# Optimization experiments

Hardware: AMD Instinct MI355X
Metric: run time of the kernel (lower is better)

Reference implementation:

```python
import jax, jax.numpy as jnp
import numpy as np

DIM = 2048
N_HEADS = 16
N_KV_HEADS = 8
HEAD_DIM = DIM // N_HEADS  # 128
N_REP = N_HEADS // N_KV_HEADS
BATCH = 2
SEQ = 2048
CHUNK = 128  # chunked-parallel causal linear attention; SEQ % CHUNK == 0


def _make_freqs_cis(seq_len, head_dim, theta=10000.0):
    freqs = 1.0 / (theta ** (np.arange(0, head_dim, 2, dtype=np.float32) / head_dim))
    t = np.arange(seq_len, dtype=np.float32)
    ang = np.outer(t, freqs)  # [S, D/2]
    return jnp.asarray(np.stack([np.cos(ang), np.sin(ang)], axis=-1))  # [S, D/2, 2]


def setup_inputs() -> dict:
    key = jax.random.key(0)
    ks = jax.random.split(key, 5)
    x = jax.random.normal(ks[0], (BATCH, SEQ, DIM), dtype=jnp.float32)
    freqs_cis = _make_freqs_cis(SEQ, HEAD_DIM)
    s = 0.02
    wq = s * jax.random.normal(ks[1], (N_HEADS * HEAD_DIM, DIM), dtype=jnp.float32)
    wk = s * jax.random.normal(ks[2], (N_KV_HEADS * HEAD_DIM, DIM), dtype=jnp.float32)
    wv = s * jax.random.normal(ks[3], (N_KV_HEADS * HEAD_DIM, DIM), dtype=jnp.float32)
    wo = s * jax.random.normal(ks[4], (DIM, N_HEADS * HEAD_DIM), dtype=jnp.float32)
    return {"x": x, "freqs_cis": freqs_cis, "wq": wq, "wk": wk, "wv": wv, "wo": wo}


def _apply_rotary(x, freqs_cis):
    # x: [B, S, H, D]; freqs_cis: [S, D/2, 2] (cos, sin). Llama pairing: (x0,x1),(x2,x3),...
    B, S, H, D = x.shape
    xr = x.reshape(B, S, H, D // 2, 2)
    x0, x1 = xr[..., 0], xr[..., 1]
    c = freqs_cis[None, :, None, :, 0]
    s = freqs_cis[None, :, None, :, 1]
    o0 = x0 * c - x1 * s
    o1 = x0 * s + x1 * c
    return jnp.stack([o0, o1], axis=-1).reshape(B, S, H, D)


def _causal_linear_attention(q, k, v):
    # q, k, v: [B, H, S, D]; output_i = q_i @ sum_{j<=i} k_j^T v_j
    B, H, S, D = q.shape
    q = jax.nn.softmax(q * (D ** -0.5), axis=-1)  # softmax over feature dim
    k = jax.nn.softmax(k, axis=2)                 # softmax over sequence dim (as in source)
    Nc = S // CHUNK
    qc = q.reshape(B, H, Nc, CHUNK, D)
    kc = k.reshape(B, H, Nc, CHUNK, D)
    vc = v.reshape(B, H, Nc, CHUNK, D)
    # per-chunk KV outer-product sums: [B, H, Nc, D, D]
    kv = jnp.einsum('bhncd,bhnce->bhnde', kc, vc)
    cum = jnp.cumsum(kv, axis=2)
    cum_excl = jnp.concatenate([jnp.zeros_like(cum[:, :, :1]), cum[:, :, :-1]], axis=2)
    inter = jnp.einsum('bhncd,bhnde->bhnce', qc, cum_excl)
    scores = jnp.einsum('bhncd,bhnmd->bhncm', qc, kc)  # [B,H,Nc,C,C]
    mask = jnp.tril(jnp.ones((CHUNK, CHUNK), dtype=bool))
    scores = jnp.where(mask, scores, jnp.zeros((), dtype=scores.dtype))
    intra = jnp.einsum('bhncm,bhnme->bhnce', scores, vc)
    return (inter + intra).reshape(B, H, S, D)


def reference(x, freqs_cis, wq, wk, wv, wo):
    B, S, _ = x.shape
    xq = (x @ wq.T).reshape(B, S, N_HEADS, HEAD_DIM)
    xk = (x @ wk.T).reshape(B, S, N_KV_HEADS, HEAD_DIM)
    xv = (x @ wv.T).reshape(B, S, N_KV_HEADS, HEAD_DIM)
    xq = _apply_rotary(xq, freqs_cis)
    xk = _apply_rotary(xk, freqs_cis)
    # repeat_kv: each kv head repeated N_REP consecutive times
    keys = jnp.repeat(xk, N_REP, axis=2)
    values = jnp.repeat(xv, N_REP, axis=2)
    q = jnp.transpose(xq, (0, 2, 1, 3))
    k = jnp.transpose(keys, (0, 2, 1, 3))
    v = jnp.transpose(values, (0, 2, 1, 3))
    out = _causal_linear_attention(q, k, v)  # [B, H, S, D]
    out = jnp.transpose(out, (0, 2, 1, 3)).reshape(B, S, N_HEADS * HEAD_DIM)
    return out @ wo.T
```

## Files before the change

kernel.cpp:

```cpp
#include <hip/hip_runtime.h>
#include <math.h>

#define DIMV 2048
#define NHEAD 16
#define NKV 8
#define HD 128
#define BATCH 2
#define SEQ 2048
#define CHUNK 128
#define NCHUNK 16
#define MTOK 4096
#define KVD (NKV * HD)

typedef _Float16 half8_t __attribute__((ext_vector_type(8)));
typedef _Float16 half4_t __attribute__((ext_vector_type(4)));
typedef _Float16 half2_t __attribute__((ext_vector_type(2)));
typedef float f32x4 __attribute__((ext_vector_type(4)));

#define GLOBAL_AS __attribute__((address_space(1)))
#define LDS_AS __attribute__((address_space(3)))

__global__ __launch_bounds__(256) void cast_all(const float* __restrict__ x,
                                                const float* __restrict__ wq,
                                                const float* __restrict__ wk,
                                                const float* __restrict__ wv,
                                                const float* __restrict__ wo,
                                                _Float16* __restrict__ xh,
                                                _Float16* __restrict__ wqkvh,
                                                _Float16* __restrict__ woh) {
  long i = (long)(blockIdx.x * 256 + threadIdx.x) * 8;
  const float* src;
  _Float16* dst;
  long off;
  if (i < 8388608)        { src = x;  dst = xh;              off = 0; }
  else if (i < 12582912)  { src = wq; dst = wqkvh;           off = 8388608; }
  else if (i < 14680064)  { src = wk; dst = wqkvh + 4194304; off = 12582912; }
  else if (i < 16777216)  { src = wv; dst = wqkvh + 6291456; off = 14680064; }
  else                    { src = wo; dst = woh;             off = 16777216; }
  long e = i - off;
  float4 a = *(const float4*)&src[e];
  float4 b = *(const float4*)&src[e + 4];
  half8_t h = {(_Float16)a.x, (_Float16)a.y, (_Float16)a.z, (_Float16)a.w,
               (_Float16)b.x, (_Float16)b.y, (_Float16)b.z, (_Float16)b.w};
  *(half8_t*)&dst[e] = h;
}

__global__ __launch_bounds__(256) void transpose_fc(const float* __restrict__ fc,
                                                    float* __restrict__ fcT) {
  __shared__ float T[64][65];
  int s0 = blockIdx.x * 64, d0 = blockIdx.y * 64;
  int t = threadIdx.x;
  int r = t >> 4, c4 = (t & 15) * 4;
#pragma unroll
  for (int p = 0; p < 4; ++p) {
    int sr = p * 16 + r;
    float4 v = *(const float4*)&fc[(size_t)(s0 + sr) * 128 + d0 + c4];
    T[sr][c4] = v.x; T[sr][c4 + 1] = v.y; T[sr][c4 + 2] = v.z; T[sr][c4 + 3] = v.w;
  }
  __syncthreads();
#pragma unroll
  for (int p = 0; p < 4; ++p) {
    int dr = p * 16 + r;
    float4 v = make_float4(T[c4][dr], T[c4 + 1][dr], T[c4 + 2][dr], T[c4 + 3][dr]);
    *(float4*)&fcT[(size_t)(d0 + dr) * SEQ + s0 + c4] = v;
  }
}

__global__ __launch_bounds__(256) void hgemm_qkv(const _Float16* __restrict__ A,
                                                 const _Float16* __restrict__ B,
                                                 const float* __restrict__ fc,
                                                 _Float16* __restrict__ qh,
                                                 _Float16* __restrict__ kT,
                                                 _Float16* __restrict__ vT) {
  const int K = 2048;
  __shared__ _Float16 As[128 * 64];
  __shared__ _Float16 Bs[128 * 64];
  __shared__ float qsum[2][128];
  const int tid = threadIdx.x;
  const int lane = tid & 63;
  const int wave = tid >> 6;
  const int row0 = blockIdx.y * 128, col0 = blockIdx.x * 128;
  const int wr = wave & 1, wc = wave >> 1;
  const int m16 = lane & 15, quad = lane >> 4;

  f32x4 acc[4][4];
#pragma unroll
  for (int i = 0; i < 4; ++i)
#pragma unroll
    for (int j = 0; j < 4; ++j) acc[i][j] = (f32x4){0.f, 0.f, 0.f, 0.f};

  const int r_ld = tid >> 3;
  const int sseg = (tid & 7) ^ (r_ld & 7);
  const size_t a_base = (size_t)(row0 + r_ld) * K + sseg * 8;
  const size_t b_base = (size_t)(col0 + r_ld) * K + sseg * 8;
  _Float16* ldsA = As + wave * 512;
  _Float16* ldsB = Bs + wave * 512;
  const int swzA = quad ^ (m16 & 7);

  for (int k0 = 0; k0 < K; k0 += 64) {
#pragma unroll
    for (int i = 0; i < 4; ++i) {
      __builtin_amdgcn_global_load_lds(
          (const GLOBAL_AS void*)(A + a_base + (size_t)i * 32 * K + k0),
          (LDS_AS void*)(ldsA + i * 2048), 16, 0, 0);
      __builtin_amdgcn_global_load_lds(
          (const GLOBAL_AS void*)(B + b_base + (size_t)i * 32 * K + k0),
          (LDS_AS void*)(ldsB + i * 2048), 16, 0, 0);
    }
    __syncthreads();
#pragma unroll
    for (int kk = 0; kk < 2; ++kk) {
      const int swz = swzA ^ (kk * 4);
      half8_t af[4], bf[4];
#pragma unroll
      for (int i = 0; i < 4; ++i) {
        af[i] = *(half8_t*)&As[(wr * 64 + i * 16 + m16) * 64 + swz * 8];
        bf[i] = *(half8_t*)&Bs[(wc * 64 + i * 16 + m16) * 64 + swz * 8];
      }
#pragma unroll
      for (int i = 0; i < 4; ++i)
#pragma unroll
        for (int j = 0; j < 4; ++j)
          acc[i][j] = __builtin_amdgcn_mfma_f32_16x16x32_f16(af[i], bf[j], acc[i][j], 0, 0, 0);
    }
    __syncthreads();
  }

  if (col0 < 2048) {
    const float sc = 0.08838834764831845f;
    float psum[4][4];
#pragma unroll
    for (int i = 0; i < 4; ++i)
#pragma unroll
      for (int r = 0; r < 4; ++r) psum[i][r] = 0.f;
#pragma unroll
    for (int i = 0; i < 4; ++i)
#pragma unroll
      for (int j = 0; j < 4; ++j) {
        int dl2 = (wc * 64 + j * 16 + m16) & ~1;
#pragma unroll
        for (int r = 0; r < 4; ++r) {
          float val = acc[i][j][r];
          float par = __shfl_xor(val, 1);
          int s_tok = (row0 + wr * 64 + i * 16 + quad * 4 + r) & (SEQ - 1);
          float2 cs = *(const float2*)&fc[(size_t)s_tok * 128 + dl2];
          float o = val * cs.x + par * ((m16 & 1) ? cs.y : -cs.y);
          float e = __expf(o * sc);
          acc[i][j][r] = e;
          psum[i][r] += e;
        }
      }
#pragma unroll
    for (int m = 1; m < 16; m <<= 1)
#pragma unroll
      for (int i = 0; i < 4; ++i)
#pragma unroll
        for (int r = 0; r < 4; ++r) psum[i][r] += __shfl_xor(psum[i][r], m);
    if (m16 == 0) {
#pragma unroll
      for (int i = 0; i < 4; ++i)
#pragma unroll
        for (int r = 0; r < 4; ++r)
          qsum[wc][wr * 64 + i * 16 + quad * 4 + r] = psum[i][r];
    }
    __syncthreads();
#pragma unroll
    for (int i = 0; i < 4; ++i)
#pragma unroll
      for (int r = 0; r < 4; ++r) {
        int rowl = wr * 64 + i * 16 + quad * 4 + r;
        psum[i][r] = 1.f / (qsum[0][rowl] + qsum[1][rowl]);
      }
#pragma unroll
    for (int i = 0; i < 4; ++i)
#pragma unroll
      for (int j = 0; j < 4; ++j) {
        int col = col0 + wc * 64 + j * 16 + m16;
#pragma unroll
        for (int r = 0; r < 4; ++r) {
          int row = row0 + wr * 64 + i * 16 + quad * 4 + r;
          qh[(size_t)row * DIMV + col] = (_Float16)(acc[i][j][r] * psum[i][r]);
        }
      }
  } else {
#pragma unroll
    for (int i = 0; i < 4; ++i)
#pragma unroll
      for (int j = 0; j < 4; ++j) {
        int col = col0 + wc * 64 + j * 16 + m16;
        int rowb = row0 + wr * 64 + i * 16 + quad * 4;
        half4_t hv = {(_Float16)acc[i][j][0], (_Float16)acc[i][j][1],
                      (_Float16)acc[i][j][2], (_Float16)acc[i][j][3]};
        if (col0 < 3072) {
          *(half4_t*)&kT[(size_t)(col - 2048) * MTOK + rowb] = hv;
        } else {
          *(half4_t*)&vT[(size_t)(col - 3072) * MTOK + rowb] = hv;
        }
      }
  }
}

__global__ __launch_bounds__(256) void hgemm_bt64_f32(const _Float16* __restrict__ A,
                                                      const _Float16* __restrict__ B,
                                                      float* __restrict__ C,
                                                      int M, int N, int K) {
  __shared__ _Float16 As[128 * 64];
  __shared__ _Float16 Bs[128 * 64];
  const int tid = threadIdx.x;
  const int lane = tid & 63;
  const int wave = tid >> 6;
  const int row0 = blockIdx.y * 128, col0 = blockIdx.x * 128;
  const int wr = wave & 1, wc = wave >> 1;
  const int m16 = lane & 15, quad = lane >> 4;

  f32x4 acc[4][4];
#pragma unroll
  for (int i = 0; i < 4; ++i)
#pragma unroll
    for (int j = 0; j < 4; ++j) acc[i][j] = (f32x4){0.f, 0.f, 0.f, 0.f};

  const int r_ld = tid >> 3;
  const int sseg = (tid & 7) ^ (r_ld & 7);
  const size_t a_base = (size_t)(row0 + r_ld) * K + sseg * 8;
  const size_t b_base = (size_t)(col0 + r_ld) * K + sseg * 8;
  _Float16* ldsA = As + wave * 512;
  _Float16* ldsB = Bs + wave * 512;
  const int swzA = quad ^ (m16 & 7);

  for (int k0 = 0; k0 < K; k0 += 64) {
#pragma unroll
    for (int i = 0; i < 4; ++i) {
      __builtin_amdgcn_global_load_lds(
          (const GLOBAL_AS void*)(A + a_base + (size_t)i * 32 * K + k0),
          (LDS_AS void*)(ldsA + i * 2048), 16, 0, 0);
      __builtin_amdgcn_global_load_lds(
          (const GLOBAL_AS void*)(B + b_base + (size_t)i * 32 * K + k0),
          (LDS_AS void*)(ldsB + i * 2048), 16, 0, 0);
    }
    __syncthreads();
#pragma unroll
    for (int kk = 0; kk < 2; ++kk) {
      const int swz = swzA ^ (kk * 4);
      half8_t af[4], bf[4];
#pragma unroll
      for (int i = 0; i < 4; ++i) {
        af[i] = *(half8_t*)&As[(wr * 64 + i * 16 + m16) * 64 + swz * 8];
        bf[i] = *(half8_t*)&Bs[(wc * 64 + i * 16 + m16) * 64 + swz * 8];
      }
#pragma unroll
      for (int i = 0; i < 4; ++i)
#pragma unroll
        for (int j = 0; j < 4; ++j)
          acc[i][j] = __builtin_amdgcn_mfma_f32_16x16x32_f16(af[i], bf[j], acc[i][j], 0, 0, 0);
    }
    __syncthreads();
  }

#pragma unroll
  for (int i = 0; i < 4; ++i)
#pragma unroll
    for (int j = 0; j < 4; ++j) {
      int col = col0 + wc * 64 + j * 16 + m16;
      int rowb = row0 + wr * 64 + i * 16 + quad * 4;
#pragma unroll
      for (int r = 0; r < 4; ++r) C[(size_t)(rowb + r) * N + col] = acc[i][j][r];
    }
}

__global__ __launch_bounds__(256) void k_rope_softmax_T(_Float16* __restrict__ kT,
                                                        const float* __restrict__ fcT) {
  int bi = blockIdx.x;
  int b = bi & 1, pr = bi >> 1;
  int d0 = pr * 2, dl = d0 & 127;
  int t = threadIdx.x;
  size_t r0 = (size_t)d0 * MTOK + b * SEQ + t * 8;
  size_t r1 = r0 + MTOK;
  half8_t x0v = *(half8_t*)&kT[r0];
  half8_t x1v = *(half8_t*)&kT[r1];
  int s8 = t * 8;
  float4 ca = *(const float4*)&fcT[(size_t)dl * SEQ + s8];
  float4 cb = *(const float4*)&fcT[(size_t)dl * SEQ + s8 + 4];
  float4 sa = *(const float4*)&fcT[(size_t)(dl + 1) * SEQ + s8];
  float4 sb = *(const float4*)&fcT[(size_t)(dl + 1) * SEQ + s8 + 4];
  float cc[8] = {ca.x, ca.y, ca.z, ca.w, cb.x, cb.y, cb.z, cb.w};
  float ss[8] = {sa.x, sa.y, sa.z, sa.w, sb.x, sb.y, sb.z, sb.w};
  float e0[8], e1[8];
  float sum0 = 0.f, sum1 = 0.f;
#pragma unroll
  for (int j = 0; j < 8; ++j) {
    float x0 = (float)x0v[j], x1 = (float)x1v[j];
    float o0 = x0 * cc[j] - x1 * ss[j];
    float o1 = x0 * ss[j] + x1 * cc[j];
    e0[j] = expf(o0); e1[j] = expf(o1);
    sum0 += e0[j]; sum1 += e1[j];
  }
#pragma unroll
  for (int off = 1; off < 64; off <<= 1) {
    sum0 += __shfl_xor(sum0, off);
    sum1 += __shfl_xor(sum1, off);
  }
  __shared__ float red[8];
  if ((t & 63) == 0) { red[(t >> 6) * 2] = sum0; red[(t >> 6) * 2 + 1] = sum1; }
  __syncthreads();
  float S0 = red[0] + red[2] + red[4] + red[6];
  float S1 = red[1] + red[3] + red[5] + red[7];
  float i0 = 1.f / S0, i1 = 1.f / S1;
  half8_t w0, w1;
#pragma unroll
  for (int j = 0; j < 8; ++j) {
    w0[j] = (_Float16)(e0[j] * i0);
    w1[j] = (_Float16)(e1[j] * i1);
  }
  *(half8_t*)&kT[r0] = w0;
  *(half8_t*)&kT[r1] = w1;
}

__global__ __launch_bounds__(256) void transpose_k(const _Float16* __restrict__ kT,
                                                   _Float16* __restrict__ kh) {
  __shared__ _Float16 T[64][65];
  int t0 = blockIdx.x * 64, d0 = blockIdx.y * 64;
  int t = threadIdx.x;
  int r = t >> 3, c8 = (t & 7) * 8;
#pragma unroll
  for (int p = 0; p < 2; ++p) {
    int dr = p * 32 + r;
    half8_t v = *(const half8_t*)&kT[(size_t)(d0 + dr) * MTOK + t0 + c8];
#pragma unroll
    for (int j = 0; j < 8; ++j) T[c8 + j][dr] = v[j];
  }
  __syncthreads();
#pragma unroll
  for (int p = 0; p < 2; ++p) {
    int tr = p * 32 + r;
    half8_t v;
#pragma unroll
    for (int j = 0; j < 8; ++j) v[j] = T[tr][c8 + j];
    *(half8_t*)&kh[(size_t)(t0 + tr) * KVD + d0 + c8] = v;
  }
}

__global__ __launch_bounds__(256) void kv_chunk_mfma(const _Float16* __restrict__ vT,
                                                     const _Float16* __restrict__ kT,
                                                     float* __restrict__ kvT) {
  __shared__ _Float16 As[128 * 32];
  __shared__ _Float16 Bs[128 * 32];
  int bi = blockIdx.x;
  int n = bi & 15, kvh = (bi >> 4) & 7, b = bi >> 7;
  int tok0 = b * SEQ + n * CHUNK;
  const int tid = threadIdx.x;
  const int lane = tid & 63;
  const int wave = tid >> 6;
  const int wr = wave & 1, wc = wave >> 1;
  const int m16 = lane & 15, quad = lane >> 4;

  f32x4 acc[4][4];
#pragma unroll
  for (int i = 0; i < 4; ++i)
#pragma unroll
    for (int j = 0; j < 4; ++j) acc[i][j] = (f32x4){0.f, 0.f, 0.f, 0.f};

  const int r_ld = tid >> 2;
  const int seg = tid & 3;
  const size_t a_base = (size_t)(kvh * HD + r_ld) * MTOK + tok0 + seg * 8;
  const size_t b_base = a_base;
  _Float16* ldsA = As + wave * 512;
  _Float16* ldsB = Bs + wave * 512;

  for (int k0 = 0; k0 < 128; k0 += 32) {
#pragma unroll
    for (int i = 0; i < 2; ++i) {
      __builtin_amdgcn_global_load_lds(
          (const GLOBAL_AS void*)(vT + a_base + (size_t)i * 64 * MTOK + k0),
          (LDS_AS void*)(ldsA + i * 2048), 16, 0, 0);
      __builtin_amdgcn_global_load_lds(
          (const GLOBAL_AS void*)(kT + b_base + (size_t)i * 64 * MTOK + k0),
          (LDS_AS void*)(ldsB + i * 2048), 16, 0, 0);
    }
    __syncthreads();
    half8_t af[4], bf[4];
#pragma unroll
    for (int i = 0; i < 4; ++i) {
      af[i] = *(half8_t*)&As[(wr * 64 + i * 16 + m16) * 32 + quad * 8];
      bf[i] = *(half8_t*)&Bs[(wc * 64 + i * 16 + m16) * 32 + quad * 8];
    }
#pragma unroll
    for (int i = 0; i < 4; ++i)
#pragma unroll
      for (int j = 0; j < 4; ++j)
        acc[i][j] = __builtin_amdgcn_mfma_f32_16x16x32_f16(af[i], bf[j], acc[i][j], 0, 0, 0);
    __syncthreads();
  }
#pragma unroll
  for (int i = 0; i < 4; ++i)
#pragma unroll
    for (int j = 0; j < 4; ++j) {
      int col = wc * 64 + j * 16 + m16;
      int rowb = wr * 64 + i * 16 + quad * 4;
#pragma unroll
      for (int r = 0; r < 4; ++r)
        kvT[(size_t)bi * 16384 + (size_t)(rowb + r) * 128 + col] = acc[i][j][r];
    }
}

__global__ __launch_bounds__(256) void cumsum_h(const float* __restrict__ kvT,
                                                _Float16* __restrict__ cumh) {
  int gid = blockIdx.x * 256 + threadIdx.x;
  int bk = gid >> 14, idx = gid & 16383;
  size_t base = (size_t)bk * NCHUNK * 16384 + idx;
  float run = 0.f;
#pragma unroll
  for (int n = 0; n < NCHUNK; ++n) {
    cumh[base + (size_t)n * 16384] = (_Float16)run;
    run += kvT[base + (size_t)n * 16384];
  }
}

__global__ __launch_bounds__(256) void attn_fused(const _Float16* __restrict__ qh,
                                                  const _Float16* __restrict__ kh,
                                                  const _Float16* __restrict__ cumh,
                                                  const _Float16* __restrict__ vT,
                                                  _Float16* __restrict__ ath) {
  __shared__ _Float16 As[128 * 32];
  __shared__ _Float16 Bs[128 * 32];
  __shared__ _Float16 Ss[128][136];
  int bi = blockIdx.x;
  int n = bi & 15, h = (bi >> 4) & 15, b = bi >> 8;
  int kvh = h >> 1;
  int tok0 = b * SEQ + n * CHUNK;
  const int tid = threadIdx.x;
  const int lane = tid & 63;
  const int wave = tid >> 6;
  const int wr = wave & 1, wc = wave >> 1;
  const int m16 = lane & 15, quad = lane >> 4;
  const int r_ld = tid >> 2;
  const int seg = tid & 3;
  _Float16* ldsA = As + wave * 512;
  _Float16* ldsB = Bs + wave * 512;

  f32x4 acc[4][4];
#pragma unroll
  for (int i = 0; i < 4; ++i)
#pragma unroll
    for (int j = 0; j < 4; ++j) acc[i][j] = (f32x4){0.f, 0.f, 0.f, 0.f};

  const size_t qbase = (size_t)(tok0 + r_ld) * DIMV + h * HD + seg * 8;
  const size_t kbase = (size_t)(tok0 + r_ld) * KVD + kvh * HD + seg * 8;
  const size_t cbase = ((size_t)((b * 8 + kvh) * 16 + n)) * 16384 + (size_t)r_ld * 128 + seg * 8;
  const size_t vbase = (size_t)(kvh * HD + r_ld) * MTOK + tok0 + seg * 8;

  for (int k0 = 0; k0 < 128; k0 += 32) {
#pragma unroll
    for (int i = 0; i < 2; ++i) {
      __builtin_amdgcn_global_load_lds(
          (const GLOBAL_AS void*)(qh + qbase + (size_t)i * 64 * DIMV + k0),
          (LDS_AS void*)(ldsA + i * 2048), 16, 0, 0);
      __builtin_amdgcn_global_load_lds(
          (const GLOBAL_AS void*)(kh + kbase + (size_t)i * 64 * KVD + k0),
          (LDS_AS void*)(ldsB + i * 2048), 16, 0, 0);
    }
    __syncthreads();
    half8_t af[4], bf[4];
#pragma unroll
    for (int i = 0; i < 4; ++i) {
      af[i] = *(half8_t*)&As[(wr * 64 + i * 16 + m16) * 32 + quad * 8];
      bf[i] = *(half8_t*)&Bs[(wc * 64 + i * 16 + m16) * 32 + quad * 8];
    }
#pragma unroll
    for (int i = 0; i < 4; ++i)
#pragma unroll
      for (int j = 0; j < 4; ++j)
        acc[i][j] = __builtin_amdgcn_mfma_f32_16x16x32_f16(af[i], bf[j], acc[i][j], 0, 0, 0);
    __syncthreads();
  }

#pragma unroll
  for (int i = 0; i < 4; ++i)
#pragma unroll
    for (int j = 0; j < 4; ++j) {
      int col = wc * 64 + j * 16 + m16;
      int rowb = wr * 64 + i * 16 + quad * 4;
#pragma unroll
      for (int r = 0; r < 4; ++r) {
        float v = (col <= rowb + r) ? acc[i][j][r] : 0.f;
        Ss[rowb + r][col] = (_Float16)v;
      }
      acc[i][j] = (f32x4){0.f, 0.f, 0.f, 0.f};
    }

  for (int ks = 0; ks < 4; ++ks) {
    int k0 = ks * 32;
#pragma unroll
    for (int i = 0; i < 2; ++i) {
      __builtin_amdgcn_global_load_lds(
          (const GLOBAL_AS void*)(qh + qbase + (size_t)i * 64 * DIMV + k0),
          (LDS_AS void*)(ldsA + i * 2048), 16, 0, 0);
      __builtin_amdgcn_global_load_lds(
          (const GLOBAL_AS void*)(cumh + cbase + (size_t)i * 64 * 128 + k0),
          (LDS_AS void*)(ldsB + i * 2048), 16, 0, 0);
    }
    __syncthreads();
    half8_t af[4], bf[4];
#pragma unroll
    for (int i = 0; i < 4; ++i) {
      af[i] = *(half8_t*)&As[(wr * 64 + i * 16 + m16) * 32 + quad * 8];
      bf[i] = *(half8_t*)&Bs[(wc * 64 + i * 16 + m16) * 32 + quad * 8];
    }
#pragma unroll
    for (int i = 0; i < 4; ++i)
#pragma unroll
      for (int j = 0; j < 4; ++j)
        acc[i][j] = __builtin_amdgcn_mfma_f32_16x16x32_f16(af[i], bf[j], acc[i][j], 0, 0, 0);
    __syncthreads();
  }

  for (int ks = 0; ks < 4; ++ks) {
    int k0 = ks * 32;
#pragma unroll
    for (int i = 0; i < 2; ++i) {
      __builtin_amdgcn_global_load_lds(
          (const GLOBAL_AS void*)(vT + vbase + (size_t)i * 64 * MTOK + k0),
          (LDS_AS void*)(ldsB + i * 2048), 16, 0, 0);
    }
    __syncthreads();
    half8_t af[4], bf[4];
#pragma unroll
    for (int i = 0; i < 4; ++i) {
      af[i] = *(half8_t*)&Ss[wr * 64 + i * 16 + m16][k0 + quad * 8];
      bf[i] = *(half8_t*)&Bs[(wc * 64 + i * 16 + m16) * 32 + quad * 8];
    }
#pragma unroll
    for (int i = 0; i < 4; ++i)
#pragma unroll
      for (int j = 0; j < 4; ++j)
        acc[i][j] = __builtin_amdgcn_mfma_f32_16x16x32_f16(af[i], bf[j], acc[i][j], 0, 0, 0);
    __syncthreads();
  }

#pragma unroll
  for (int i = 0; i < 4; ++i)
#pragma unroll
    for (int j = 0; j < 4; ++j) {
      int col = wc * 64 + j * 16 + m16;
      int rowb = wr * 64 + i * 16 + quad * 4;
#pragma unroll
      for (int r = 0; r < 4; ++r)
        ath[(size_t)(tok0 + rowb + r) * DIMV + h * HD + col] = (_Float16)acc[i][j][r];
    }
}

extern "C" void kernel_launch(void* const* d_in, const int* in_sizes, int n_in,
                              void* d_out, int out_size, void* d_ws, size_t ws_size,
                              hipStream_t stream) {
  const float* x  = (const float*)d_in[0];
  const float* fc = (const float*)d_in[1];
  const float* wq = (const float*)d_in[2];
  const float* wk = (const float*)d_in[3];
  const float* wv = (const float*)d_in[4];
  const float* wo = (const float*)d_in[5];
  float* out = (float*)d_out;

  char* p = (char*)d_ws;
  _Float16* xh    = (_Float16*)p;  p += 16777216;
  _Float16* wqkvh = (_Float16*)p;  p += 16777216;
  _Float16* woh   = (_Float16*)p;  p += 8388608;
  _Float16* qh    = (_Float16*)p;  p += 16777216;
  _Float16* kT    = (_Float16*)p;  p += 8388608;
  _Float16* kh    = (_Float16*)p;  p += 8388608;
  _Float16* vT    = (_Float16*)p;  p += 8388608;
  float*    kvT   = (float*)p;     p += 16777216;
  _Float16* cumh  = (_Float16*)p;  p += 8388608;
  _Float16* ath   = (_Float16*)p;  p += 16777216;
  float*    fcT   = (float*)p;     p += 1048576;

  cast_all<<<10240, 256, 0, stream>>>(x, wq, wk, wv, wo, xh, wqkvh, woh);
  transpose_fc<<<dim3(32, 2), 256, 0, stream>>>(fc, fcT);

  hgemm_qkv<<<dim3(32, 32), 256, 0, stream>>>(xh, wqkvh, fc, qh, kT, vT);

  k_rope_softmax_T<<<1024, 256, 0, stream>>>(kT, fcT);
  transpose_k<<<dim3(64, 16), 256, 0, stream>>>(kT, kh);

  kv_chunk_mfma<<<256, 256, 0, stream>>>(vT, kT, kvT);
  cumsum_h<<<1024, 256, 0, stream>>>(kvT, cumh);
  attn_fused<<<512, 256, 0, stream>>>(qh, kh, cumh, vT, ath);

  hgemm_bt64_f32<<<dim3(16, 32), 256, 0, stream>>>(ath, woh, out, MTOK, 2048, 2048);
}
```

Measured before the change: 298.0 us.

## Rewrite QKV GEMM as 256x256 tile with 8-wave double-buffered ping-pong pipeline

```diff
diff --git a/kernel.cpp b/kernel.cpp
--- a/kernel.cpp
+++ b/kernel.cpp
@@ -66,131 +66,187 @@
   }
 }
 
-__global__ __launch_bounds__(256) void hgemm_qkv(const _Float16* __restrict__ A,
-                                                 const _Float16* __restrict__ B,
-                                                 const float* __restrict__ fc,
-                                                 _Float16* __restrict__ qh,
-                                                 _Float16* __restrict__ kT,
-                                                 _Float16* __restrict__ vT) {
+#define BARX() __builtin_amdgcn_s_barrier()
+#define WAITL0() asm volatile("s_waitcnt lgkmcnt(0)" ::: "memory")
+#define WAITVM(n) asm volatile("s_waitcnt vmcnt(" #n ")" ::: "memory")
+
+#define STG_A(bb, kk, i, k0)                                                      \
+  __builtin_amdgcn_global_load_lds(                                               \
+      (const GLOBAL_AS void*)(A + aoff + (size_t)(i) * 128 * 2048 + (k0) + (kk) * 32), \
+      (LDS_AS void*)(As + ((bb) * 2 + (kk)) * 8192 + (i) * 4096 + wave * 512), 16, 0, 0)
+#define STG_B(bb, kk, i, k0)                                                      \
+  __builtin_amdgcn_global_load_lds(                                               \
+      (const GLOBAL_AS void*)(B + boff + (size_t)(i) * 128 * 2048 + (k0) + (kk) * 32), \
+      (LDS_AS void*)(Bs + ((bb) * 2 + (kk)) * 8192 + (i) * 4096 + wave * 512), 16, 0, 0)
+
+#define LDA_F(bb, kk, ih) do {                                                    \
+    const _Float16* pA_ = As + ((bb) * 2 + (kk)) * 8192 +                         \
+                          (wr * 128 + (ih) * 64 + m16) * 32 + pseg8;              \
+    af[0] = *(const half8_t*)(pA_);                                               \
+    af[1] = *(const half8_t*)(pA_ + 512);                                         \
+    af[2] = *(const half8_t*)(pA_ + 1024);                                        \
+    af[3] = *(const half8_t*)(pA_ + 1536);                                        \
+  } while (0)
+#define LDB_F(bb, kk) do {                                                        \
+    const _Float16* pB_ = Bs + ((bb) * 2 + (kk)) * 8192 +                         \
+                          (wc * 64 + m16) * 32 + pseg8;                           \
+    bf[0] = *(const half8_t*)(pB_);                                               \
+    bf[1] = *(const half8_t*)(pB_ + 512);                                         \
+    bf[2] = *(const half8_t*)(pB_ + 1024);                                        \
+    bf[3] = *(const half8_t*)(pB_ + 1536);                                        \
+  } while (0)
+
+#define MMX(ih) do {                                                              \
+    _Pragma("unroll")                                                             \
+    for (int i_ = 0; i_ < 4; ++i_)                                                \
+      _Pragma("unroll")                                                           \
+      for (int j_ = 0; j_ < 4; ++j_)                                              \
+        acc[(ih) * 4 + i_][j_] = __builtin_amdgcn_mfma_f32_16x16x32_f16(          \
+            af[i_], bf[j_], acc[(ih) * 4 + i_][j_], 0, 0, 0);                     \
+  } while (0)
+
+#define KTILE(bb, k0, DS1, DS2, DS3, DS4, VA, VB) do {                            \
+  half8_t af[4], bf[4];                                                           \
+                                                           \
+  LDA_F(bb, 0, 0); LDB_F(bb, 0);                                                  \
+  if (DS1) { STG_A(1 - (bb), 1, 0, (k0) + 64); STG_A(1 - (bb), 1, 1, (k0) + 64); } \
+  BARX(); WAITL0();                                                               \
+  __builtin_amdgcn_s_setprio(1); MMX(0); __builtin_amdgcn_s_setprio(0);           \
+  BARX();                                                                         \
+                                                \
+  LDA_F(bb, 0, 1);                                                                \
+  if (DS2) { STG_B(1 - (bb), 1, 0, (k0) + 64); STG_B(1 - (bb), 1, 1, (k0) + 64); } \
+  WAITVM(VA);                                                                     \
+  BARX(); WAITL0();                                                               \
+  __builtin_amdgcn_s_setprio(1); MMX(1); __builtin_amdgcn_s_setprio(0);           \
+  BARX();                                                                         \
+                                                           \
+  LDA_F(bb, 1, 0); LDB_F(bb, 1);                                                  \
+  if (DS3) { STG_A(bb, 0, 0, (k0) + 128); STG_A(bb, 0, 1, (k0) + 128); }          \
+  BARX(); WAITL0();                                                               \
+  __builtin_amdgcn_s_setprio(1); MMX(0); __builtin_amdgcn_s_setprio(0);           \
+  BARX();                                                                         \
+                                                \
+  LDA_F(bb, 1, 1);                                                                \
+  if (DS4) { STG_B(bb, 0, 0, (k0) + 128); STG_B(bb, 0, 1, (k0) + 128); }          \
+  WAITVM(VB);                                                                     \
+  BARX(); WAITL0();                                                               \
+  __builtin_amdgcn_s_setprio(1); MMX(1); __builtin_amdgcn_s_setprio(0);           \
+  BARX();                                                                         \
+} while (0)
+
+__global__ __launch_bounds__(512, 2) void hgemm_qkv_8p(const _Float16* __restrict__ A,
+                                                       const _Float16* __restrict__ B,
+                                                       const float* __restrict__ fc,
+                                                       _Float16* __restrict__ qh,
+                                                       _Float16* __restrict__ kT,
+                                                       _Float16* __restrict__ vT) {
   const int K = 2048;
-  __shared__ _Float16 As[128 * 64];
-  __shared__ _Float16 Bs[128 * 64];
-  __shared__ float qsum[2][128];
+  __shared__ _Float16 As[32768];
+  __shared__ _Float16 Bs[32768];
+  __shared__ float qsum[4][256];
+
   const int tid = threadIdx.x;
   const int lane = tid & 63;
   const int wave = tid >> 6;
-  const int row0 = blockIdx.y * 128, col0 = blockIdx.x * 128;
-  const int wr = wave & 1, wc = wave >> 1;
+  const int wr = wave >> 2;
+  const int wc = wave & 3;
   const int m16 = lane & 15, quad = lane >> 4;
-
-  f32x4 acc[4][4];
-#pragma unroll
-  for (int i = 0; i < 4; ++i)
-#pragma unroll
-    for (int j = 0; j < 4; ++j) acc[i][j] = (f32x4){0.f, 0.f, 0.f, 0.f};
-
-  const int r_ld = tid >> 3;
-  const int sseg = (tid & 7) ^ (r_ld & 7);
-  const size_t a_base = (size_t)(row0 + r_ld) * K + sseg * 8;
-  const size_t b_base = (size_t)(col0 + r_ld) * K + sseg * 8;
-  _Float16* ldsA = As + wave * 512;
-  _Float16* ldsB = Bs + wave * 512;
-  const int swzA = quad ^ (m16 & 7);
-
-  for (int k0 = 0; k0 < K; k0 += 64) {
-#pragma unroll
-    for (int i = 0; i < 4; ++i) {
-      __builtin_amdgcn_global_load_lds(
-          (const GLOBAL_AS void*)(A + a_base + (size_t)i * 32 * K + k0),
-          (LDS_AS void*)(ldsA + i * 2048), 16, 0, 0);
-      __builtin_amdgcn_global_load_lds(
-          (const GLOBAL_AS void*)(B + b_base + (size_t)i * 32 * K + k0),
-          (LDS_AS void*)(ldsB + i * 2048), 16, 0, 0);
-    }
-    __syncthreads();
-#pragma unroll
-    for (int kk = 0; kk < 2; ++kk) {
-      const int swz = swzA ^ (kk * 4);
-      half8_t af[4], bf[4];
-#pragma unroll
-      for (int i = 0; i < 4; ++i) {
-        af[i] = *(half8_t*)&As[(wr * 64 + i * 16 + m16) * 64 + swz * 8];
-        bf[i] = *(half8_t*)&Bs[(wc * 64 + i * 16 + m16) * 64 + swz * 8];
-      }
-#pragma unroll
-      for (int i = 0; i < 4; ++i)
-#pragma unroll
-        for (int j = 0; j < 4; ++j)
-          acc[i][j] = __builtin_amdgcn_mfma_f32_16x16x32_f16(af[i], bf[j], acc[i][j], 0, 0, 0);
-    }
-    __syncthreads();
-  }
+  const int row0 = blockIdx.y * 256, col0 = blockIdx.x * 256;
+  const int pseg8 = (quad ^ (m16 & 3)) * 8;
+
+  const int r_ld = tid >> 2;
+  const int sseg = (tid & 3) ^ (r_ld & 3);
+  const size_t aoff = (size_t)(row0 + r_ld) * K + sseg * 8;
+  const size_t boff = (size_t)(col0 + r_ld) * K + sseg * 8;
+
+  f32x4 acc[8][4];
+#pragma unroll
+  for (int m = 0; m < 8; ++m)
+#pragma unroll
+    for (int j = 0; j < 4; ++j) acc[m][j] = (f32x4){0.f, 0.f, 0.f, 0.f};
+
+  STG_A(0, 0, 0, 0); STG_A(0, 0, 1, 0); STG_B(0, 0, 0, 0); STG_B(0, 0, 1, 0);
+  STG_A(0, 1, 0, 0); STG_A(0, 1, 1, 0); STG_B(0, 1, 0, 0); STG_B(0, 1, 1, 0);
+  STG_A(1, 0, 0, 64); STG_A(1, 0, 1, 64); STG_B(1, 0, 0, 64); STG_B(1, 0, 1, 64);
+  WAITVM(8);
+  BARX();
+
+  for (int t = 0; t < 30; t += 2) {
+    KTILE(0, t * 64,      1, 1, 1, 1, 8, 8);
+    KTILE(1, t * 64 + 64, 1, 1, 1, 1, 8, 8);
+  }
+  KTILE(0, 1920, 1, 1, 0, 0, 8, 4);
+  KTILE(1, 1984, 0, 0, 0, 0, 0, 0);
 
   if (col0 < 2048) {
     const float sc = 0.08838834764831845f;
-    float psum[4][4];
-#pragma unroll
-    for (int i = 0; i < 4; ++i)
-#pragma unroll
-      for (int r = 0; r < 4; ++r) psum[i][r] = 0.f;
-#pragma unroll
-    for (int i = 0; i < 4; ++i)
+    float psum[8][4];
+#pragma unroll
+    for (int m = 0; m < 8; ++m)
+#pragma unroll
+      for (int r = 0; r < 4; ++r) psum[m][r] = 0.f;
+#pragma unroll
+    for (int m = 0; m < 8; ++m)
 #pragma unroll
       for (int j = 0; j < 4; ++j) {
-        int dl2 = (wc * 64 + j * 16 + m16) & ~1;
+        int dl2 = (wc * 64 + j * 16 + m16) & 126;
 #pragma unroll
         for (int r = 0; r < 4; ++r) {
-          float val = acc[i][j][r];
+          float val = acc[m][j][r];
           float par = __shfl_xor(val, 1);
-          int s_tok = (row0 + wr * 64 + i * 16 + quad * 4 + r) & (SEQ - 1);
+          int row_l = wr * 128 + (m >> 2) * 64 + (m & 3) * 16 + quad * 4 + r;
+          int s_tok = (row0 + row_l) & (SEQ - 1);
           float2 cs = *(const float2*)&fc[(size_t)s_tok * 128 + dl2];
           float o = val * cs.x + par * ((m16 & 1) ? cs.y : -cs.y);
           float e = __expf(o * sc);
-          acc[i][j][r] = e;
-          psum[i][r] += e;
+          acc[m][j][r] = e;
+          psum[m][r] += e;
         }
       }
 #pragma unroll
-    for (int m = 1; m < 16; m <<= 1)
-#pragma unroll
-      for (int i = 0; i < 4; ++i)
-#pragma unroll
-        for (int r = 0; r < 4; ++r) psum[i][r] += __shfl_xor(psum[i][r], m);
+    for (int mm = 1; mm < 16; mm <<= 1)
+#pragma unroll
+      for (int m = 0; m < 8; ++m)
+#pragma unroll
+        for (int r = 0; r < 4; ++r) psum[m][r] += __shfl_xor(psum[m][r], mm);
     if (m16 == 0) {
 #pragma unroll
-      for (int i = 0; i < 4; ++i)
-#pragma unroll
-        for (int r = 0; r < 4; ++r)
-          qsum[wc][wr * 64 + i * 16 + quad * 4 + r] = psum[i][r];
-    }
-    __syncthreads();
-#pragma unroll
-    for (int i = 0; i < 4; ++i)
+      for (int m = 0; m < 8; ++m)
+#pragma unroll
+        for (int r = 0; r < 4; ++r) {
+          int row_l = wr * 128 + (m >> 2) * 64 + (m & 3) * 16 + quad * 4 + r;
+          qsum[wc][row_l] = psum[m][r];
+        }
+    }
+    __syncthreads();
+#pragma unroll
+    for (int m = 0; m < 8; ++m)
 #pragma unroll
       for (int r = 0; r < 4; ++r) {
-        int rowl = wr * 64 + i * 16 + quad * 4 + r;
-        psum[i][r] = 1.f / (qsum[0][rowl] + qsum[1][rowl]);
+        int row_l = wr * 128 + (m >> 2) * 64 + (m & 3) * 16 + quad * 4 + r;
+        psum[m][r] = 1.f / (qsum[wc & 2][row_l] + qsum[(wc & 2) | 1][row_l]);
       }
 #pragma unroll
-    for (int i = 0; i < 4; ++i)
+    for (int m = 0; m < 8; ++m)
 #pragma unroll
       for (int j = 0; j < 4; ++j) {
         int col = col0 + wc * 64 + j * 16 + m16;
 #pragma unroll
         for (int r = 0; r < 4; ++r) {
-          int row = row0 + wr * 64 + i * 16 + quad * 4 + r;
-          qh[(size_t)row * DIMV + col] = (_Float16)(acc[i][j][r] * psum[i][r]);
+          int row_l = wr * 128 + (m >> 2) * 64 + (m & 3) * 16 + quad * 4 + r;
+          qh[(size_t)(row0 + row_l) * DIMV + col] = (_Float16)(acc[m][j][r] * psum[m][r]);
         }
       }
   } else {
 #pragma unroll
-    for (int i = 0; i < 4; ++i)
+    for (int m = 0; m < 8; ++m)
 #pragma unroll
       for (int j = 0; j < 4; ++j) {
         int col = col0 + wc * 64 + j * 16 + m16;
-        int rowb = row0 + wr * 64 + i * 16 + quad * 4;
-        half4_t hv = {(_Float16)acc[i][j][0], (_Float16)acc[i][j][1],
-                      (_Float16)acc[i][j][2], (_Float16)acc[i][j][3]};
+        int rowb = row0 + wr * 128 + (m >> 2) * 64 + (m & 3) * 16 + quad * 4;
+        half4_t hv = {(_Float16)acc[m][j][0], (_Float16)acc[m][j][1],
+                      (_Float16)acc[m][j][2], (_Float16)acc[m][j][3]};
         if (col0 < 3072) {
           *(half4_t*)&kT[(size_t)(col - 2048) * MTOK + rowb] = hv;
         } else {
@@ -575,7 +631,7 @@
   cast_all<<<10240, 256, 0, stream>>>(x, wq, wk, wv, wo, xh, wqkvh, woh);
   transpose_fc<<<dim3(32, 2), 256, 0, stream>>>(fc, fcT);
 
-  hgemm_qkv<<<dim3(32, 32), 256, 0, stream>>>(xh, wqkvh, fc, qh, kT, vT);
+  hgemm_qkv_8p<<<dim3(16, 16), 512, 0, stream>>>(xh, wqkvh, fc, qh, kT, vT);
 
   k_rope_softmax_T<<<1024, 256, 0, stream>>>(kT, fcT);
   transpose_k<<<dim3(64, 16), 256, 0, stream>>>(kT, kh);
```

After: 294.4 us. No clear change (-1.2%).
